# Kernel tuning notes

Hardware: AMD Instinct MI355X
Metric: run time of the kernel (lower is better)

The kernel has to match this reference:

```python
import jax, jax.numpy as jnp
import numpy as np

BN_EPS = 1e-5


def setup_inputs() -> dict:
    key = jax.random.key(0)
    ks = jax.random.split(key, 11)
    B, C, Ci, D, H, W = 2, 256, 128, 8, 32, 32
    s = 0.02  # weight init scale
    return {
        "x": jax.random.normal(ks[0], (B, C, D, H, W), dtype=jnp.float32),
        "Wt": jax.random.normal(ks[1], (Ci, C), dtype=jnp.float32) * s,
        "bt": jax.random.normal(ks[2], (Ci,), dtype=jnp.float32) * s,
        "Wp": jax.random.normal(ks[3], (Ci, C), dtype=jnp.float32) * s,
        "bp": jax.random.normal(ks[4], (Ci,), dtype=jnp.float32) * s,
        "Wg": jax.random.normal(ks[5], (Ci, C), dtype=jnp.float32) * s,
        "bg": jax.random.normal(ks[6], (Ci,), dtype=jnp.float32) * s,
        "Ww": jax.random.normal(ks[7], (C, Ci), dtype=jnp.float32) * s,
        "bw": jax.random.normal(ks[8], (C,), dtype=jnp.float32) * s,
        "gamma": jax.random.normal(ks[9], (C,), dtype=jnp.float32),
        "beta": jax.random.normal(ks[10], (C,), dtype=jnp.float32),
    }


def reference(x, Wt, bt, Wp, bp, Wg, bg, Ww, bw, gamma, beta):
    # x: [B, C, D, H, W]; 1x1x1 Conv3d == per-position channel GEMM.
    B, C, D, H, W = x.shape
    xf = x.reshape(B, C, -1)  # [B, C, N], N = D*H*W

    theta = jnp.einsum('oc,bcn->bno', Wt, xf) + bt          # [B, N, Ci]
    phi = jnp.einsum('oc,bcn->bon', Wp, xf) + bp[None, :, None]  # [B, Ci, N]
    g = jnp.einsum('oc,bcn->bno', Wg, xf) + bg              # [B, N, Ci]

    # Unscaled, unmasked full self-attention over all N spatial positions.
    f = jnp.einsum('bnc,bcm->bnm', theta, phi)              # [B, N, N]
    a = jax.nn.softmax(f, axis=-1)
    y = jnp.einsum('bnm,bmc->bcn', a, g)                    # [B, Ci, N]

    # Output projection W: conv1x1 then BatchNorm3d (training-mode batch stats).
    wy = jnp.einsum('oc,bcn->bon', Ww, y) + bw[None, :, None]  # [B, C, N]
    mean = jnp.mean(wy, axis=(0, 2), keepdims=True)
    var = jnp.var(wy, axis=(0, 2), keepdims=True)
    wy_bn = (wy - mean) * jax.lax.rsqrt(var + BN_EPS)
    wy_bn = wy_bn * gamma[None, :, None] + beta[None, :, None]

    return wy_bn.reshape(B, C, D, H, W) + x
```

## Files before the change

kernel.cpp:

```cpp
#include <hip/hip_runtime.h>
#include <cstdint>
#include <cstddef>


typedef unsigned short u16;
typedef __bf16 bf16x8 __attribute__((ext_vector_type(8)));
typedef float f32x4 __attribute__((ext_vector_type(4)));
typedef float f32x16 __attribute__((ext_vector_type(16)));
typedef unsigned short u16x8 __attribute__((ext_vector_type(8)));

#define B_ 2
#define C_ 256
#define CI_ 128
#define N_ 8192
#define CHUNKS 4
#define CHUNK_N 2048
#define KVB 64
#define NT (CHUNK_N/KVB)

static __device__ __forceinline__ u16 f2bf(float f){
  unsigned u = __builtin_bit_cast(unsigned, f);
  unsigned r = (u + 0x7FFFu + ((u>>16)&1u)) >> 16;
  return (u16)r;
}
static __device__ __forceinline__ float bf2f(u16 v){
  unsigned u = ((unsigned)v) << 16;
  return __builtin_bit_cast(float, u);
}
static __device__ __forceinline__ f32x4 f4zero(){
  f32x4 v; v[0]=0.f; v[1]=0.f; v[2]=0.f; v[3]=0.f; return v;
}
static __device__ __forceinline__ f32x16 f16zero(){
  f32x16 v;
#pragma unroll
  for (int i=0;i<16;i++) v[i]=0.f;
  return v;
}
static __device__ __forceinline__ f32x4 mfma16(bf16x8 a, bf16x8 b, f32x4 c){
  return __builtin_amdgcn_mfma_f32_16x16x32_bf16(a, b, c, 0, 0, 0);
}
static __device__ __forceinline__ f32x16 mfma32(bf16x8 a, bf16x8 b, f32x16 c){
  return __builtin_amdgcn_mfma_f32_32x32x16_bf16(a, b, c, 0, 0, 0);
}
static __device__ __forceinline__ unsigned cvtpk(float lo, float hi){
  unsigned r;
  asm("v_cvt_pk_bf16_f32 %0, %1, %2" : "=v"(r) : "v"(lo), "v"(hi));
  return r;
}
static __device__ __forceinline__ void plswap(unsigned &a, unsigned &b){
  asm volatile("v_permlane32_swap_b32 %0, %1" : "+v"(a), "+v"(b));
}

__global__ void k0_prep(const float* __restrict__ Wt, const float* __restrict__ Wp,
                        const float* __restrict__ Wg, const float* __restrict__ Ww,
                        const float* __restrict__ bt, const float* __restrict__ bp,
                        const float* __restrict__ bg,
                        u16* __restrict__ Wcat, u16* __restrict__ Wwb,
                        float* __restrict__ biasc, float* __restrict__ stats){
  int t = blockIdx.x*blockDim.x + threadIdx.x;
  int nthr = gridDim.x*blockDim.x;
  for (int i = t; i < 32768; i += nthr){
    Wcat[i]        = f2bf(Wt[i]);
    Wcat[32768+i]  = f2bf(Wp[i]);
    Wcat[65536+i]  = f2bf(Wg[i]);
    Wwb[i]         = f2bf(Ww[i]);
  }
  for (int i = t; i < 128; i += nthr){
    biasc[i] = bt[i]; biasc[128+i] = bp[i]; biasc[256+i] = bg[i];
  }
  for (int i = t; i < 512; i += nthr) stats[i] = 0.f;
}

__global__ __launch_bounds__(256) void k1_proj(const float* __restrict__ x,
     const u16* __restrict__ Wcat, const float* __restrict__ biasc,
     u16* __restrict__ theta, u16* __restrict__ kproj, u16* __restrict__ gT){
  __shared__ u16 At[64*264];
  __shared__ u16 Wt_[32*264];
  __shared__ u16 gbuf[32*72];
  int tid = threadIdx.x;
  int b  = blockIdx.x >> 7;
  int nb = (blockIdx.x & 127) * 64;
  int w = tid >> 6, lane = tid & 63;
  int l15 = lane & 15, kg = lane >> 4;

  {
    int cp = tid & 127, nh = tid >> 7;
    int c0 = cp*2;
    const float* src0 = x + ((size_t)(b*C_ + c0))*N_ + nb + nh*32;
    const float* src1 = src0 + N_;
#pragma unroll
    for (int j=0;j<8;j++){
      f32x4 a = *(const f32x4*)(src0 + j*4);
      f32x4 c = *(const f32x4*)(src1 + j*4);
#pragma unroll
      for (int q=0;q<4;q++){
        unsigned pk = (unsigned)f2bf(a[q]) | ((unsigned)f2bf(c[q])<<16);
        *(unsigned*)&At[(nh*32 + j*4 + q)*264 + c0] = pk;
      }
    }
  }
  __syncthreads();

  bf16x8 afr[8];
#pragma unroll
  for (int kc=0;kc<8;kc++)
    afr[kc] = *(const bf16x8*)&At[(w*16+l15)*264 + kc*32 + kg*8];

  for (int och = 0; och < 12; och++){
    {
      int o8 = tid>>3, cp8 = tid&7;
      const u16* wsrc = Wcat + ((size_t)(och*32 + o8))*256 + cp8*8;
#pragma unroll
      for (int j=0;j<4;j++)
        *(u16x8*)&Wt_[o8*264 + cp8*8 + j*64] = *(const u16x8*)(wsrc + j*64);
    }
    __syncthreads();

    f32x4 acc0 = f4zero(), acc1 = f4zero();
#pragma unroll
    for (int kc=0;kc<8;kc++){
      bf16x8 b0 = *(const bf16x8*)&Wt_[(l15)*264 + kc*32 + kg*8];
      bf16x8 b1 = *(const bf16x8*)&Wt_[(16+l15)*264 + kc*32 + kg*8];
      acc0 = mfma16(afr[kc], b0, acc0);
      acc1 = mfma16(afr[kc], b1, acc1);
    }

    if (och < 8){
      u16* dst = (och < 4) ? theta : kproj;
      int oo = (och & 3) * 32;
#pragma unroll
      for (int of=0;of<2;of++){
        int o = oo + of*16 + l15;
        float bias = biasc[och*32 + of*16 + l15];
        f32x4 acc = of ? acc1 : acc0;
#pragma unroll
        for (int i=0;i<4;i++){
          int n = nb + w*16 + kg*4 + i;
          dst[((size_t)b*N_ + n)*CI_ + o] = f2bf(acc[i] + bias);
        }
      }
      __syncthreads();
    } else {
#pragma unroll
      for (int of=0;of<2;of++){
        int o = of*16 + l15;
        float bias = biasc[och*32 + of*16 + l15];
        f32x4 acc = of ? acc1 : acc0;
#pragma unroll
        for (int i=0;i<4;i++){
          int r = w*16 + kg*4 + i;
          gbuf[o*72 + r] = f2bf(acc[i] + bias);
        }
      }
      __syncthreads();
      {
        int o = tid>>3, np = tid&7;
        int og = (och-8)*32 + o;
        u16x8 v = *(const u16x8*)&gbuf[o*72 + np*8];
        *(u16x8*)(gT + ((size_t)b*CI_ + og)*N_ + nb + np*8) = v;
      }
      __syncthreads();
    }
  }
}

__global__ __launch_bounds__(512, 2) void k2_attn(const u16* __restrict__ theta,
      const u16* __restrict__ kproj, const u16* __restrict__ gT,
      u16* __restrict__ pO, float* __restrict__ pM, float* __restrict__ pL){
  __shared__ char smem[65536];
  char* kbase = smem;
  char* vbase = smem + 32768;
  int tid = threadIdx.x;
  int bid = blockIdx.x;
  int combo = bid & 7;
  int b = combo & 1;
  int chunk = combo >> 1;
  int qblk = bid >> 3;
  int n0 = chunk * CHUNK_N;
  int w = tid >> 6, lane = tid & 63;
  int l31 = lane & 31, hi = lane >> 5;
  int qg = qblk*256 + w*32 + l31;

  bf16x8 qf[8];
  {
    const u16* qsrc = theta + ((size_t)b*N_ + qg)*CI_ + hi*8;
#pragma unroll
    for (int cc=0; cc<8; cc++) qf[cc] = *(const bf16x8*)(qsrc + cc*16);
  }

  int krow_s = tid >> 3, kpart = tid & 7;
  int vrow_s = tid >> 2, vpart = tid & 3;
  const u16* ksrc = kproj + ((size_t)b*N_ + n0 + krow_s)*CI_ + kpart*16;
  const u16* vsrc = gT + ((size_t)b*CI_ + vrow_s)*N_ + n0 + vpart*16;
  int kw_off[2], vw_off[2];
#pragma unroll
  for (int j=0;j<2;j++){
    int cb = kpart*32 + j*16;
    kw_off[j] = krow_s*256 + (cb ^ ((krow_s&7)<<4));
    int kb = vpart*32 + j*16;
    vw_off[j] = vrow_s*128 + (kb ^ ((vrow_s&7)<<4));
  }
  int swz = (l31&7)<<4;
  int kro[8], vro[4];
#pragma unroll
  for (int cc=0;cc<8;cc++) kro[cc] = l31*256 + ((cc*32 + hi*16) ^ swz);
#pragma unroll
  for (int ks=0;ks<4;ks++) vro[ks] = l31*128 + ((ks*32 + hi*16) ^ swz);

#pragma unroll
  for (int j=0;j<2;j++){
    *(u16x8*)(kbase + kw_off[j]) = *(const u16x8*)(ksrc + j*8);
    *(u16x8*)(vbase + vw_off[j]) = *(const u16x8*)(vsrc + j*8);
  }
  __syncthreads();

  f32x16 oacc[4];
#pragma unroll
  for (int i=0;i<4;i++) oacc[i] = f16zero();
  float mrun = -1e30f, lrun = 0.f;

  for (int t=0; t<NT; t++){
    int cur = t & 1;
    char* kb_c = kbase + cur*16384;
    char* vb_c = vbase + cur*16384;
    u16x8 kst[2], vst[2];
    bool pf = (t+1 < NT);
    if (pf){
      const u16* ks = ksrc + (size_t)(t+1)*KVB*CI_;
      const u16* vs = vsrc + (t+1)*KVB;
#pragma unroll
      for (int j=0;j<2;j++) kst[j] = *(const u16x8*)(ks + j*8);
#pragma unroll
      for (int j=0;j<2;j++) vst[j] = *(const u16x8*)(vs + j*8);
    }

    f32x16 sA = f16zero(), sB = f16zero();
    __builtin_amdgcn_s_setprio(1);
#pragma unroll
    for (int cc=0; cc<8; cc++){
      bf16x8 kf0 = *(const bf16x8*)(kb_c + kro[cc]);
      bf16x8 kf1 = *(const bf16x8*)(kb_c + 8192 + kro[cc]);
      sA = mfma32(kf0, qf[cc], sA);
      sB = mfma32(kf1, qf[cc], sB);
    }
    __builtin_amdgcn_s_setprio(0);

    float t8[8];
#pragma unroll
    for (int i=0;i<8;i++) t8[i] = fmaxf(fmaxf(sA[i], sA[i+8]), fmaxf(sB[i], sB[i+8]));
    float m4a = fmaxf(t8[0], t8[4]), m4b = fmaxf(t8[1], t8[5]);
    float m4c = fmaxf(t8[2], t8[6]), m4d = fmaxf(t8[3], t8[7]);
    float mx = fmaxf(fmaxf(m4a, m4b), fmaxf(m4c, m4d));
    mx = fmaxf(mx, __shfl_xor(mx, 32));
    if (__any(mx > mrun + 8.f)){
      float mnew = fmaxf(mrun, mx);
      float sc = __expf(mrun - mnew);
      lrun *= sc;
#pragma unroll
      for (int i=0;i<4;i++)
#pragma unroll
        for (int r=0;r<16;r++) oacc[i][r] *= sc;
      mrun = mnew;
    }
    float pA[16], pB[16];
#pragma unroll
    for (int r=0;r<16;r++){ pA[r] = __expf(sA[r]-mrun); pB[r] = __expf(sB[r]-mrun); }
    float s8[8];
#pragma unroll
    for (int i=0;i<8;i++) s8[i] = (pA[i]+pA[i+8]) + (pB[i]+pB[i+8]);
    float s4a = s8[0]+s8[4], s4b = s8[1]+s8[5], s4c = s8[2]+s8[6], s4d = s8[3]+s8[7];
    float ps = (s4a+s4b) + (s4c+s4d);
    ps += __shfl_xor(ps, 32);
    lrun += ps;

    if (pf){
      char* kd = kbase + (cur^1)*16384;
      char* vd = vbase + (cur^1)*16384;
#pragma unroll
      for (int j=0;j<2;j++) *(u16x8*)(kd + kw_off[j]) = kst[j];
#pragma unroll
      for (int j=0;j<2;j++) *(u16x8*)(vd + vw_off[j]) = vst[j];
    }

    __builtin_amdgcn_s_setprio(1);
#pragma unroll
    for (int ks=0; ks<4; ks++){
      const float* P = (ks<2) ? pA : pB;
      int r0 = (ks&1)*8;
      unsigned a0 = cvtpk(P[r0+0], P[r0+1]);
      unsigned b0 = cvtpk(P[r0+4], P[r0+5]);
      unsigned a1 = cvtpk(P[r0+2], P[r0+3]);
      unsigned b1 = cvtpk(P[r0+6], P[r0+7]);
      plswap(a0, b0); plswap(a1, b1);
      union { unsigned u[4]; bf16x8 v; } pb;
      pb.u[0]=a0; pb.u[1]=a1; pb.u[2]=b0; pb.u[3]=b1;
#pragma unroll
      for (int c2=0; c2<4; c2++){
        bf16x8 vf = *(const bf16x8*)(vb_c + c2*4096 + vro[ks]);
        oacc[c2] = mfma32(vf, pb.v, oacc[c2]);
      }
    }
    __builtin_amdgcn_s_setprio(0);
    __syncthreads();
  }

  char* region = smem + w*8192;
#pragma unroll
  for (int c2=0;c2<4;c2++)
#pragma unroll
    for (int r=0;r<16;r++){
      int c = c2*32 + (r&3) + 8*(r>>2) + 4*hi;
      *(u16*)(region + l31*256 + ((c*2) ^ swz)) = f2bf(oacc[c2][r]);
    }
  __syncthreads();
  {
    int ql = lane >> 1, half = lane & 1;
    int qg2 = qblk*256 + w*32 + ql;
    u16* dst = pO + ((size_t)(chunk*2 + b)*N_ + qg2)*CI_ + half*64;
    int rswz = (ql&7)<<4;
#pragma unroll
    for (int j=0;j<8;j++){
      u16x8 v2 = *(const u16x8*)(region + ql*256 + ((half*128 + j*16) ^ rswz));
      *(u16x8*)(dst + j*8) = v2;
    }
  }
  if (hi == 0){
    pM[(size_t)(chunk*2 + b)*N_ + qg] = mrun;
    pL[(size_t)(chunk*2 + b)*N_ + qg] = lrun;
  }
}

__global__ __launch_bounds__(256) void k2b_combine(const u16* __restrict__ pO,
    const float* __restrict__ pM, const float* __restrict__ pL,
    float* __restrict__ y){
  int tid = threadIdx.x;
  int blk = blockIdx.x;
  int b = blk >> 9;
  int q = (blk & 511) * 16 + (tid >> 4);
  int c0 = (tid & 15) * 8;
  size_t qi = (size_t)b*N_ + q;
  float m0 = pM[qi], m1 = pM[2*(size_t)N_ + qi], m2 = pM[4*(size_t)N_ + qi], m3 = pM[6*(size_t)N_ + qi];
  float M = fmaxf(fmaxf(m0,m1), fmaxf(m2,m3));
  float w0 = __expf(m0-M), w1 = __expf(m1-M), w2 = __expf(m2-M), w3 = __expf(m3-M);
  float L = w0*pL[qi] + w1*pL[2*(size_t)N_+qi] + w2*pL[4*(size_t)N_+qi] + w3*pL[6*(size_t)N_+qi];
  float inv = 1.f/L;
  float wts[4] = {w0,w1,w2,w3};
  float acc[8];
#pragma unroll
  for (int i=0;i<8;i++) acc[i]=0.f;
  const u16* src = pO + qi*CI_ + c0;
#pragma unroll
  for (int ch=0; ch<4; ch++){
    u16x8 v = *(const u16x8*)(src + (size_t)ch*2*N_*CI_);
#pragma unroll
    for (int i=0;i<8;i++) acc[i] += wts[ch]*bf2f(v[i]);
  }
  float* dst = y + qi*CI_ + c0;
  f32x4 o0, o1;
#pragma unroll
  for (int i=0;i<4;i++){ o0[i] = acc[i]*inv; o1[i] = acc[4+i]*inv; }
  *(f32x4*)dst = o0;
  *(f32x4*)(dst+4) = o1;
}

__global__ __launch_bounds__(256) void k3_wy(const float* __restrict__ y,
    const u16* __restrict__ Wwb, const float* __restrict__ bw,
    float* __restrict__ wy, float* __restrict__ stats){
  __shared__ u16 Yt[64*136];
  __shared__ u16 Wt_[64*136];
  __shared__ float wyb[64*72];
  int tid = threadIdx.x;
  int b  = blockIdx.x >> 7;
  int nb = (blockIdx.x & 127) * 64;
  int w = tid>>6, lane = tid&63;
  int l15 = lane&15, kg = lane>>4;

  {
    int n = tid>>2, cp = tid&3;
    const float* src = y + ((size_t)b*N_ + nb + n)*CI_ + cp*32;
#pragma unroll
    for (int j=0;j<8;j++){
      f32x4 v = *(const f32x4*)(src + j*4);
      unsigned p0 = (unsigned)f2bf(v[0]) | ((unsigned)f2bf(v[1])<<16);
      unsigned p1 = (unsigned)f2bf(v[2]) | ((unsigned)f2bf(v[3])<<16);
      *(unsigned*)&Yt[n*136 + cp*32 + j*4]     = p0;
      *(unsigned*)&Yt[n*136 + cp*32 + j*4 + 2] = p1;
    }
  }
  __syncthreads();

  bf16x8 afr[4];
#pragma unroll
  for (int kc=0;kc<4;kc++)
    afr[kc] = *(const bf16x8*)&Yt[(w*16+l15)*136 + kc*32 + kg*8];

  for (int oc=0; oc<4; oc++){
    {
      int o = tid>>2, cp = tid&3;
      const u16* src = Wwb + ((size_t)(oc*64 + o))*CI_ + cp*32;
#pragma unroll
      for (int j=0;j<4;j++)
        *(u16x8*)&Wt_[o*136 + cp*32 + j*8] = *(const u16x8*)(src + j*8);
    }
    __syncthreads();

    f32x4 acc[4];
#pragma unroll
    for (int of=0;of<4;of++) acc[of] = f4zero();
#pragma unroll
    for (int kc=0;kc<4;kc++){
#pragma unroll
      for (int of=0;of<4;of++){
        bf16x8 bfr = *(const bf16x8*)&Wt_[(of*16+l15)*136 + kc*32 + kg*8];
        acc[of] = mfma16(afr[kc], bfr, acc[of]);
      }
    }
#pragma unroll
    for (int of=0;of<4;of++){
#pragma unroll
      for (int i=0;i<4;i++)
        wyb[(of*16+l15)*72 + w*16 + kg*4 + i] = acc[of][i];
    }
    __syncthreads();
    {
      int o = tid>>2, np = tid&3;
      int og = oc*64 + o;
      float bias = bw[og];
      float sm = 0.f, sq = 0.f;
      float* dst = wy + ((size_t)b*C_ + og)*N_ + nb + np*16;
#pragma unroll
      for (int j=0;j<4;j++){
        f32x4 v;
#pragma unroll
        for (int q=0;q<4;q++){
          float t2 = wyb[o*72 + np*16 + j*4 + q] + bias;
          v[q] = t2; sm += t2; sq += t2*t2;
        }
        *(f32x4*)(dst + j*4) = v;
      }
      sm += __shfl_xor(sm, 1); sm += __shfl_xor(sm, 2);
      sq += __shfl_xor(sq, 1); sq += __shfl_xor(sq, 2);
      if ((tid&3)==0){
        atomicAdd(&stats[og], sm);
        atomicAdd(&stats[256+og], sq);
      }
    }
    __syncthreads();
  }
}

__global__ __launch_bounds__(256) void k4_bn(const float* __restrict__ wy,
    const float* __restrict__ x, const float* __restrict__ stats,
    const float* __restrict__ gamma, const float* __restrict__ beta,
    float* __restrict__ out){
  size_t base = ((size_t)blockIdx.x)*2048 + (size_t)threadIdx.x*8;
  int o = (int)((base >> 13) & 255);
  const float invn = 1.f/16384.f;
  float mean = stats[o]*invn;
  float var  = stats[256+o]*invn - mean*mean;
  float rs = rsqrtf(var + 1e-5f);
  float g = gamma[o]*rs;
  float bb = beta[o];
  f32x4 a0 = *(const f32x4*)(wy + base);
  f32x4 a1 = *(const f32x4*)(wy + base + 4);
  f32x4 x0 = *(const f32x4*)(x + base);
  f32x4 x1 = *(const f32x4*)(x + base + 4);
  f32x4 r0, r1;
#pragma unroll
  for (int q=0;q<4;q++){
    r0[q] = (a0[q]-mean)*g + bb + x0[q];
    r1[q] = (a1[q]-mean)*g + bb + x1[q];
  }
  *(f32x4*)(out + base)     = r0;
  *(f32x4*)(out + base + 4) = r1;
}

extern "C" void kernel_launch(void* const* d_in, const int* in_sizes, int n_in,
                              void* d_out, int out_size, void* d_ws, size_t ws_size,
                              hipStream_t stream){
  const float* x     = (const float*)d_in[0];
  const float* Wt    = (const float*)d_in[1];
  const float* bt    = (const float*)d_in[2];
  const float* Wp    = (const float*)d_in[3];
  const float* bp    = (const float*)d_in[4];
  const float* Wg    = (const float*)d_in[5];
  const float* bg    = (const float*)d_in[6];
  const float* Ww    = (const float*)d_in[7];
  const float* bw    = (const float*)d_in[8];
  const float* gamma = (const float*)d_in[9];
  const float* beta  = (const float*)d_in[10];

  char* ws = (char*)d_ws;
  u16*   theta = (u16*)(ws + 0);
  u16*   kproj = (u16*)(ws + 4194304);
  u16*   gT    = (u16*)(ws + 8388608);
  u16*   pO    = (u16*)(ws + 12582912);
  float* pM    = (float*)(ws + 29360128);
  float* pL    = (float*)(ws + 29622272);
  u16*   Wcat  = (u16*)(ws + 29884416);
  u16*   Wwb   = (u16*)(ws + 30081024);
  float* biasc = (float*)(ws + 30146560);
  float* stats = (float*)(ws + 30148096);
  float* y     = (float*)(ws + 0);
  float* wy    = (float*)(ws + 12582912);
  float* out   = (float*)d_out;

  k0_prep<<<64, 256, 0, stream>>>(Wt, Wp, Wg, Ww, bt, bp, bg, Wcat, Wwb, biasc, stats);
  k1_proj<<<256, 256, 0, stream>>>(x, Wcat, biasc, theta, kproj, gT);
  k2_attn<<<256, 512, 0, stream>>>(theta, kproj, gT, pO, pM, pL);
  k2b_combine<<<1024, 256, 0, stream>>>(pO, pM, pL, y);
  k3_wy<<<256, 256, 0, stream>>>(y, Wwb, bw, wy, stats);
  k4_bn<<<2048, 256, 0, stream>>>(wy, x, stats, gamma, beta, out);
}
```

Measured before the change: 144.2 us.

## Split attention KV into 8 chunks when workspace allows, use exp2 softmax

Templates the attention and combine kernels on the number of key/value split chunks. When the workspace is large enough it launches 8 chunks (512 blocks) instead of 4, so the grid fills more of the GPU's compute units. Launch bounds are raised to allow 4 blocks per SM. Theta weights and bias are pre-scaled by log2(e) so the softmax can use exp2 instead of exp, and the rescale threshold is loosened from 8 to 12. The trade-off is more partial-output traffic and a larger combine step.

```diff
diff --git a/kernel.cpp b/kernel.cpp
--- a/kernel.cpp
+++ b/kernel.cpp
@@ -13,10 +13,7 @@
 #define C_ 256
 #define CI_ 128
 #define N_ 8192
-#define CHUNKS 4
-#define CHUNK_N 2048
 #define KVB 64
-#define NT (CHUNK_N/KVB)
 
 static __device__ __forceinline__ u16 f2bf(float f){
   unsigned u = __builtin_bit_cast(unsigned, f);
@@ -50,6 +47,8 @@
 static __device__ __forceinline__ void plswap(unsigned &a, unsigned &b){
   asm volatile("v_permlane32_swap_b32 %0, %1" : "+v"(a), "+v"(b));
 }
+
+#define LOG2E 1.4426950408889634f
 
 __global__ void k0_prep(const float* __restrict__ Wt, const float* __restrict__ Wp,
                         const float* __restrict__ Wg, const float* __restrict__ Ww,
@@ -60,13 +59,13 @@
   int t = blockIdx.x*blockDim.x + threadIdx.x;
   int nthr = gridDim.x*blockDim.x;
   for (int i = t; i < 32768; i += nthr){
-    Wcat[i]        = f2bf(Wt[i]);
+    Wcat[i]        = f2bf(Wt[i] * LOG2E);
     Wcat[32768+i]  = f2bf(Wp[i]);
     Wcat[65536+i]  = f2bf(Wg[i]);
     Wwb[i]         = f2bf(Ww[i]);
   }
   for (int i = t; i < 128; i += nthr){
-    biasc[i] = bt[i]; biasc[128+i] = bp[i]; biasc[256+i] = bg[i];
+    biasc[i] = bt[i] * LOG2E; biasc[128+i] = bp[i]; biasc[256+i] = bg[i];
   }
   for (int i = t; i < 512; i += nthr) stats[i] = 0.f;
 }
@@ -164,18 +163,21 @@
   }
 }
 
-__global__ __launch_bounds__(512, 2) void k2_attn(const u16* __restrict__ theta,
+template<int CH>
+__global__ __launch_bounds__(512, 4) void k2_attn(const u16* __restrict__ theta,
       const u16* __restrict__ kproj, const u16* __restrict__ gT,
       u16* __restrict__ pO, float* __restrict__ pM, float* __restrict__ pL){
+  constexpr int CHUNK_N = N_ / CH;
+  constexpr int NTI = CHUNK_N / KVB;
   __shared__ char smem[65536];
   char* kbase = smem;
   char* vbase = smem + 32768;
   int tid = threadIdx.x;
   int bid = blockIdx.x;
-  int combo = bid & 7;
+  int combo = bid & (2*CH - 1);
   int b = combo & 1;
   int chunk = combo >> 1;
-  int qblk = bid >> 3;
+  int qblk = bid / (2*CH);
   int n0 = chunk * CHUNK_N;
   int w = tid >> 6, lane = tid & 63;
   int l31 = lane & 31, hi = lane >> 5;
@@ -219,12 +221,12 @@
   for (int i=0;i<4;i++) oacc[i] = f16zero();
   float mrun = -1e30f, lrun = 0.f;
 
-  for (int t=0; t<NT; t++){
+  for (int t=0; t<NTI; t++){
     int cur = t & 1;
     char* kb_c = kbase + cur*16384;
     char* vb_c = vbase + cur*16384;
     u16x8 kst[2], vst[2];
-    bool pf = (t+1 < NT);
+    bool pf = (t+1 < NTI);
     if (pf){
       const u16* ks = ksrc + (size_t)(t+1)*KVB*CI_;
       const u16* vs = vsrc + (t+1)*KVB;
@@ -252,9 +254,9 @@
     float m4c = fmaxf(t8[2], t8[6]), m4d = fmaxf(t8[3], t8[7]);
     float mx = fmaxf(fmaxf(m4a, m4b), fmaxf(m4c, m4d));
     mx = fmaxf(mx, __shfl_xor(mx, 32));
-    if (__any(mx > mrun + 8.f)){
+    if (__any(mx > mrun + 12.f)){
       float mnew = fmaxf(mrun, mx);
-      float sc = __expf(mrun - mnew);
+      float sc = exp2f(mrun - mnew);
       lrun *= sc;
 #pragma unroll
       for (int i=0;i<4;i++)
@@ -264,7 +266,7 @@
     }
     float pA[16], pB[16];
 #pragma unroll
-    for (int r=0;r<16;r++){ pA[r] = __expf(sA[r]-mrun); pB[r] = __expf(sB[r]-mrun); }
+    for (int r=0;r<16;r++){ pA[r] = exp2f(sA[r]-mrun); pB[r] = exp2f(sB[r]-mrun); }
     float s8[8];
 #pragma unroll
     for (int i=0;i<8;i++) s8[i] = (pA[i]+pA[i+8]) + (pB[i]+pB[i+8]);
@@ -330,6 +332,7 @@
   }
 }
 
+template<int CH>
 __global__ __launch_bounds__(256) void k2b_combine(const u16* __restrict__ pO,
     const float* __restrict__ pM, const float* __restrict__ pL,
     float* __restrict__ y){
@@ -339,18 +342,26 @@
   int q = (blk & 511) * 16 + (tid >> 4);
   int c0 = (tid & 15) * 8;
   size_t qi = (size_t)b*N_ + q;
-  float m0 = pM[qi], m1 = pM[2*(size_t)N_ + qi], m2 = pM[4*(size_t)N_ + qi], m3 = pM[6*(size_t)N_ + qi];
-  float M = fmaxf(fmaxf(m0,m1), fmaxf(m2,m3));
-  float w0 = __expf(m0-M), w1 = __expf(m1-M), w2 = __expf(m2-M), w3 = __expf(m3-M);
-  float L = w0*pL[qi] + w1*pL[2*(size_t)N_+qi] + w2*pL[4*(size_t)N_+qi] + w3*pL[6*(size_t)N_+qi];
+  float m[CH], l[CH];
+#pragma unroll
+  for (int ch=0; ch<CH; ch++){
+    m[ch] = pM[(size_t)(ch*2)*N_ + qi];
+    l[ch] = pL[(size_t)(ch*2)*N_ + qi];
+  }
+  float M = m[0];
+#pragma unroll
+  for (int ch=1; ch<CH; ch++) M = fmaxf(M, m[ch]);
+  float wts[CH];
+  float L = 0.f;
+#pragma unroll
+  for (int ch=0; ch<CH; ch++){ wts[ch] = exp2f(m[ch]-M); L += wts[ch]*l[ch]; }
   float inv = 1.f/L;
-  float wts[4] = {w0,w1,w2,w3};
   float acc[8];
 #pragma unroll
   for (int i=0;i<8;i++) acc[i]=0.f;
   const u16* src = pO + qi*CI_ + c0;
 #pragma unroll
-  for (int ch=0; ch<4; ch++){
+  for (int ch=0; ch<CH; ch++){
     u16x8 v = *(const u16x8*)(src + (size_t)ch*2*N_*CI_);
 #pragma unroll
     for (int i=0;i<8;i++) acc[i] += wts[ch]*bf2f(v[i]);
@@ -490,25 +501,36 @@
   const float* gamma = (const float*)d_in[9];
   const float* beta  = (const float*)d_in[10];
 
+  const size_t BIG_NEED = 47451648;
+  bool big = (ws_size >= BIG_NEED);
+
   char* ws = (char*)d_ws;
   u16*   theta = (u16*)(ws + 0);
   u16*   kproj = (u16*)(ws + 4194304);
   u16*   gT    = (u16*)(ws + 8388608);
   u16*   pO    = (u16*)(ws + 12582912);
-  float* pM    = (float*)(ws + 29360128);
-  float* pL    = (float*)(ws + 29622272);
-  u16*   Wcat  = (u16*)(ws + 29884416);
-  u16*   Wwb   = (u16*)(ws + 30081024);
-  float* biasc = (float*)(ws + 30146560);
-  float* stats = (float*)(ws + 30148096);
+  size_t po_bytes = big ? (size_t)33554432 : (size_t)16777216;
+  char*  tail  = ws + 12582912 + po_bytes;
+  float* pM    = (float*)(tail);
+  size_t ml_bytes = big ? (size_t)524288 : (size_t)262144;
+  float* pL    = (float*)(tail + ml_bytes);
+  u16*   Wcat  = (u16*)(tail + 2*ml_bytes);
+  u16*   Wwb   = (u16*)(tail + 2*ml_bytes + 196608);
+  float* biasc = (float*)(tail + 2*ml_bytes + 262144);
+  float* stats = (float*)(tail + 2*ml_bytes + 263680);
   float* y     = (float*)(ws + 0);
   float* wy    = (float*)(ws + 12582912);
   float* out   = (float*)d_out;
 
   k0_prep<<<64, 256, 0, stream>>>(Wt, Wp, Wg, Ww, bt, bp, bg, Wcat, Wwb, biasc, stats);
   k1_proj<<<256, 256, 0, stream>>>(x, Wcat, biasc, theta, kproj, gT);
-  k2_attn<<<256, 512, 0, stream>>>(theta, kproj, gT, pO, pM, pL);
-  k2b_combine<<<1024, 256, 0, stream>>>(pO, pM, pL, y);
+  if (big){
+    k2_attn<8><<<512, 512, 0, stream>>>(theta, kproj, gT, pO, pM, pL);
+    k2b_combine<8><<<1024, 256, 0, stream>>>(pO, pM, pL, y);
+  } else {
+    k2_attn<4><<<256, 512, 0, stream>>>(theta, kproj, gT, pO, pM, pL);
+    k2b_combine<4><<<1024, 256, 0, stream>>>(pO, pM, pL, y);
+  }
   k3_wy<<<256, 256, 0, stream>>>(y, Wwb, bw, wy, stats);
   k4_bn<<<2048, 256, 0, stream>>>(wy, x, stats, gamma, beta, out);
 }
```

New measurement: 301.0 us. 2.09x slower.
